# Kernel tuning notes

Hardware: AMD Instinct MI355X
Metric: run time of the kernel (lower is better)

Reference implementation:

```python
import jax, jax.numpy as jnp
import numpy as np

DIM_IN = 768
DIM_OUT = 64
SEQ = 4096
BATCH = 4

def setup_inputs() -> dict:
    key = jax.random.key(0)
    ks = jax.random.split(key, 7)
    s = 1.0 / np.sqrt(DIM_IN)
    return {
        "x": jax.random.normal(ks[0], (BATCH, SEQ, DIM_IN), dtype=jnp.float32),
        "wq": jax.random.uniform(ks[1], (DIM_IN, DIM_OUT), jnp.float32, -s, s),
        "bq": jax.random.uniform(ks[2], (DIM_OUT,), jnp.float32, -s, s),
        "wk": jax.random.uniform(ks[3], (DIM_IN, DIM_OUT), jnp.float32, -s, s),
        "bk": jax.random.uniform(ks[4], (DIM_OUT,), jnp.float32, -s, s),
        "wv": jax.random.uniform(ks[5], (DIM_IN, DIM_OUT), jnp.float32, -s, s),
        "bv": jax.random.uniform(ks[6], (DIM_OUT,), jnp.float32, -s, s),
    }

def reference(x, wq, bq, wk, bk, wv, bv):
    # QKV projections: (B, S, D_in) @ (D_in, D_out) + bias
    q = x @ wq + bq
    k = x @ wk + bk
    v = x @ wv + bv
    # full causal attention, scores scaled by sqrt(d_out) AFTER masking (as in source)
    scores = jnp.einsum('bqd,bkd->bqk', q, k)  # (B, S, S)
    seq = x.shape[1]
    causal = jnp.tril(jnp.ones((seq, seq), dtype=bool))  # True = keep
    scores = jnp.where(causal, scores, -jnp.inf)
    scale = 1.0 / np.sqrt(k.shape[-1]).astype(np.float32)
    weights = jax.nn.softmax(scores * scale, axis=-1)
    # dropout_rate = 0.0 -> identity
    return jnp.einsum('bqk,bkd->bqd', weights, v)
```

## Files before the change

### kernel.cpp

```cpp
#include <hip/hip_runtime.h>
#include <hip/hip_bf16.h>

#define BATCH 4
#define SEQ   4096
#define DIN   768
#define DOUT  64

typedef __attribute__((ext_vector_type(4))) float f32x4;
typedef __attribute__((ext_vector_type(8))) short short8;
typedef __attribute__((ext_vector_type(4))) short short4v;
typedef __attribute__((ext_vector_type(2))) unsigned uint2v;

#define QSCALE 0.18033688011112043f

static __device__ __forceinline__ unsigned short f2bf(float f) {
    union { float f; unsigned u; } un; un.f = f;
    unsigned r = un.u + 0x7FFF + ((un.u >> 16) & 1);
    return (unsigned short)(r >> 16);
}
static __device__ __forceinline__ float bf2f(unsigned short h) {
    union { unsigned u; float f; } un; un.u = ((unsigned)h) << 16;
    return un.f;
}
static __device__ __forceinline__ unsigned packbf(float lo, float hi) {
    return ((unsigned)f2bf(hi) << 16) | (unsigned)f2bf(lo);
}

__global__ void wprep_kernel(const float* __restrict__ wq,
                             const float* __restrict__ wk,
                             const float* __restrict__ wv,
                             unsigned short* __restrict__ wF) {
    __shared__ float lds[64][65];
    int o = blockIdx.x / 12, kt = blockIdx.x % 12;
    const float* w = (o == 0) ? wq : (o == 1) ? wk : wv;
    int tid = threadIdx.x;
    int k0 = kt * 64;
    #pragma unroll
    for (int i = 0; i < 16; ++i) {
        int flat = tid + i * 256;
        int kl = flat >> 6, n = flat & 63;
        lds[kl][n] = w[(k0 + kl) * 64 + n];
    }
    __syncthreads();
    int lane = tid & 63;
    int m = lane & 15, g = lane >> 4;
    #pragma unroll
    for (int i = 0; i < 2; ++i) {
        int f = i * 4 + (tid >> 6);
        int t = f >> 1, kcl = f & 1;
        int kc = kt * 2 + kcl;
        int nc = o * 4 + t;
        short8 v;
        #pragma unroll
        for (int j = 0; j < 8; ++j)
            v[j] = (short)f2bf(lds[kcl * 32 + g * 8 + j][t * 16 + m]);
        *(short8*)&wF[(size_t)(nc * 24 + kc) * 512 + lane * 8] = v;
    }
}

__global__ void __launch_bounds__(256) proj_kernel(
        const float* __restrict__ x,
        const float* __restrict__ bq,
        const float* __restrict__ bk,
        const float* __restrict__ bv,
        const unsigned short* __restrict__ wF,
        unsigned short* __restrict__ Qf,
        unsigned short* __restrict__ Kf,
        unsigned short* __restrict__ Vf) {
    __shared__ __align__(16) unsigned short xs[32][776];
    __shared__ unsigned short tr[4][16][24];

    int tid = threadIdx.x;
    int w = tid >> 6;
    int lane = tid & 63;
    int m = lane & 15, g = lane >> 4;
    int r0 = blockIdx.x * 32;

    {
        const float* xbase = x + (size_t)r0 * DIN;
        #pragma unroll
        for (int i = 0; i < 24; ++i) {
            int flat4 = tid + i * 256;
            int row = flat4 / 192;
            int c4 = flat4 - row * 192;
            float4 v = *(const float4*)(xbase + (size_t)row * DIN + c4 * 4);
            short4v sv;
            sv[0] = (short)f2bf(v.x); sv[1] = (short)f2bf(v.y);
            sv[2] = (short)f2bf(v.z); sv[3] = (short)f2bf(v.w);
            *(short4v*)&xs[row][c4 * 4] = sv;
        }
    }
    __syncthreads();

    f32x4 acc[2][3];
    #pragma unroll
    for (int st = 0; st < 2; ++st)
        #pragma unroll
        for (int t = 0; t < 3; ++t) acc[st][t] = (f32x4){0.f, 0.f, 0.f, 0.f};

    const unsigned short* wb0 = wF + (size_t)((w * 3 + 0) * 24) * 512 + lane * 8;
    const unsigned short* wb1 = wF + (size_t)((w * 3 + 1) * 24) * 512 + lane * 8;
    const unsigned short* wb2 = wF + (size_t)((w * 3 + 2) * 24) * 512 + lane * 8;

    short8 bf0 = *(const short8*)(wb0);
    short8 bf1 = *(const short8*)(wb1);
    short8 bf2 = *(const short8*)(wb2);
    short8 af0 = *(const short8*)&xs[m][g * 8];
    short8 af1 = *(const short8*)&xs[16 + m][g * 8];

    for (int kc = 0; kc < 24; ++kc) {
        short8 nb0, nb1, nb2, na0, na1;
        bool have = (kc + 1) < 24;
        if (have) {
            int off = (kc + 1) * 512;
            nb0 = *(const short8*)(wb0 + off);
            nb1 = *(const short8*)(wb1 + off);
            nb2 = *(const short8*)(wb2 + off);
            na0 = *(const short8*)&xs[m][(kc + 1) * 32 + g * 8];
            na1 = *(const short8*)&xs[16 + m][(kc + 1) * 32 + g * 8];
        }
        acc[0][0] = __builtin_amdgcn_mfma_f32_16x16x32_bf16(af0, bf0, acc[0][0], 0, 0, 0);
        acc[1][0] = __builtin_amdgcn_mfma_f32_16x16x32_bf16(af1, bf0, acc[1][0], 0, 0, 0);
        acc[0][1] = __builtin_amdgcn_mfma_f32_16x16x32_bf16(af0, bf1, acc[0][1], 0, 0, 0);
        acc[1][1] = __builtin_amdgcn_mfma_f32_16x16x32_bf16(af1, bf1, acc[1][1], 0, 0, 0);
        acc[0][2] = __builtin_amdgcn_mfma_f32_16x16x32_bf16(af0, bf2, acc[0][2], 0, 0, 0);
        acc[1][2] = __builtin_amdgcn_mfma_f32_16x16x32_bf16(af1, bf2, acc[1][2], 0, 0, 0);
        if (have) {
            bf0 = nb0; bf1 = nb1; bf2 = nb2;
            af0 = na0; af1 = na1;
        }
    }

    int b2 = r0 >> 12;
    int s = (r0 & 4095) >> 5;
    #pragma unroll
    for (int st = 0; st < 2; ++st) {
        #pragma unroll
        for (int tt = 0; tt < 3; ++tt) {
            int nc = w * 3 + tt;
            int o = nc >> 2;
            int t = nc & 3;
            const float* bias_p = (o == 0) ? bq : (o == 1) ? bk : bv;
            float bias = bias_p[t * 16 + m];
            #pragma unroll
            for (int r = 0; r < 4; ++r) {
                float val = acc[st][tt][r] + bias;
                if (o == 0) val *= QSCALE;
                tr[w][g * 4 + r][m] = f2bf(val);
            }
            if (o < 2) {
                if (g < 2) {
                    short8 v8;
                    #pragma unroll
                    for (int j = 0; j < 8; ++j) v8[j] = (short)tr[w][m][g * 8 + j];
                    unsigned short* dst = (o == 0) ? Qf : Kf;
                    int c = t >> 1;
                    *(short8*)&dst[(size_t)((blockIdx.x * 2 + st) * 2 + c) * 512
                                   + (((t & 1) * 2 + g) * 16 + m) * 8] = v8;
                }
            } else {
                if (g < 2) {
                    short8 v8;
                    #pragma unroll
                    for (int j = 0; j < 8; ++j) v8[j] = (short)tr[w][g * 8 + j][m];
                    *(short8*)&Vf[((size_t)(b2 * 128 + s) * 4 + t) * 512
                                  + ((st * 2 + g) * 16 + m) * 8] = v8;
                }
            }
        }
    }
}

__global__ void __launch_bounds__(512, 1) attn_kernel(
        const unsigned short* __restrict__ Qf,
        const unsigned short* __restrict__ Kf,
        const unsigned short* __restrict__ Vf,
        float* __restrict__ out) {
    __shared__ __align__(16) unsigned short PT[8][16][40];
    __shared__ __align__(16) unsigned short pacc[8][16][68];
    __shared__ float pm[8][16];
    __shared__ float pl[8][16];

    int j = blockIdx.x;
    int b = j & 3;
    int qt = j >> 2;
    int T[4];
    T[0] = qt; T[1] = 127 - qt; T[2] = 128 + qt; T[3] = 255 - qt;
    int ns[4], base[4];
    #pragma unroll
    for (int i = 0; i < 4; ++i) { base[i] = T[i] * 16; ns[i] = (T[i] + 2) >> 1; }
    int tid = threadIdx.x;
    int w = tid >> 6;
    int lane = tid & 63;
    int m = lane & 15, g = lane >> 4;

    short8 qfr[4][2];
    #pragma unroll
    for (int i = 0; i < 4; ++i) {
        const unsigned short* Qp = Qf + (size_t)(b * 256 + T[i]) * 1024 + lane * 8;
        qfr[i][0] = *(const short8*)(Qp);
        qfr[i][1] = *(const short8*)(Qp + 512);
    }

    short8 onesA;
    #pragma unroll
    for (int jj = 0; jj < 8; ++jj) onesA[jj] = (short)0x3F80;

    f32x4 acc[4][5];
    #pragma unroll
    for (int rt = 0; rt < 4; ++rt)
        #pragma unroll
        for (int t = 0; t < 5; ++t) acc[rt][t] = (f32x4){0.f, 0.f, 0.f, 0.f};
    float mrun[4];
    #pragma unroll
    for (int rt = 0; rt < 4; ++rt) mrun[rt] = -INFINITY;

    const unsigned short* Kbase = Kf + (size_t)(b * 256) * 1024 + lane * 8;
    const unsigned short* Vbase = Vf + (size_t)(b * 128) * 2048 + lane * 8;

    short8 kf[4], vf[4];
    if (w < ns[3]) {
        #pragma unroll
        for (int t = 0; t < 4; ++t) {
            kf[t] = *(const short8*)(Kbase + (size_t)w * 2048 + t * 512);
            vf[t] = *(const short8*)(Vbase + (size_t)w * 2048 + t * 512);
        }
    }

    for (int s = w; s < ns[3]; s += 8) {
        int kv0 = s * 32;
        int sn = s + 8;
        bool have = (sn < ns[3]);

        #pragma unroll
        for (int rt = 0; rt < 4; ++rt) {
            if (rt < 3 && s >= ns[rt]) continue;

            f32x4 st0 = (f32x4){0.f, 0.f, 0.f, 0.f};
            f32x4 st1 = (f32x4){0.f, 0.f, 0.f, 0.f};
            st0 = __builtin_amdgcn_mfma_f32_16x16x32_bf16(kf[0], qfr[rt][0], st0, 0, 0, 0);
            st0 = __builtin_amdgcn_mfma_f32_16x16x32_bf16(kf[1], qfr[rt][1], st0, 0, 0, 0);
            st1 = __builtin_amdgcn_mfma_f32_16x16x32_bf16(kf[2], qfr[rt][0], st1, 0, 0, 0);
            st1 = __builtin_amdgcn_mfma_f32_16x16x32_bf16(kf[3], qfr[rt][1], st1, 0, 0, 0);

            if (rt == 3 && have) {
                #pragma unroll
                for (int t = 0; t < 4; ++t)
                    kf[t] = *(const short8*)(Kbase + (size_t)sn * 2048 + t * 512);
            }

            if (s == ns[rt] - 1) {
                int q = base[rt] + m;
                #pragma unroll
                for (int r = 0; r < 4; ++r) {
                    if (kv0 + g * 4 + r > q)      st0[r] = -INFINITY;
                    if (kv0 + 16 + g * 4 + r > q) st1[r] = -INFINITY;
                }
            }

            float th = mrun[rt] + 8.0f;
            bool need = (st0[0] > th) | (st0[1] > th) | (st0[2] > th) | (st0[3] > th)
                      | (st1[0] > th) | (st1[1] > th) | (st1[2] > th) | (st1[3] > th);
            if (__any(need)) {
                float rmax = fmaxf(fmaxf(fmaxf(st0[0], st0[1]), fmaxf(st0[2], st0[3])),
                                   fmaxf(fmaxf(st1[0], st1[1]), fmaxf(st1[2], st1[3])));
                rmax = fmaxf(rmax, __shfl_xor(rmax, 16));
                rmax = fmaxf(rmax, __shfl_xor(rmax, 32));
                float mnew = fmaxf(mrun[rt], rmax);
                float alpha = __builtin_amdgcn_exp2f(mrun[rt] - mnew);
                mrun[rt] = mnew;
                #pragma unroll
                for (int t = 0; t < 5; ++t)
                    #pragma unroll
                    for (int r = 0; r < 4; ++r) acc[rt][t][r] *= alpha;
            }
            float p00 = __builtin_amdgcn_exp2f(st0[0] - mrun[rt]);
            float p01 = __builtin_amdgcn_exp2f(st0[1] - mrun[rt]);
            float p02 = __builtin_amdgcn_exp2f(st0[2] - mrun[rt]);
            float p03 = __builtin_amdgcn_exp2f(st0[3] - mrun[rt]);
            float p10 = __builtin_amdgcn_exp2f(st1[0] - mrun[rt]);
            float p11 = __builtin_amdgcn_exp2f(st1[1] - mrun[rt]);
            float p12 = __builtin_amdgcn_exp2f(st1[2] - mrun[rt]);
            float p13 = __builtin_amdgcn_exp2f(st1[3] - mrun[rt]);
            *(uint2v*)&PT[w][m][g * 4]      = (uint2v){packbf(p00, p01), packbf(p02, p03)};
            *(uint2v*)&PT[w][m][16 + g * 4] = (uint2v){packbf(p10, p11), packbf(p12, p13)};
            short8 pb = *(const short8*)&PT[w][m][g * 8];
            #pragma unroll
            for (int t = 0; t < 4; ++t)
                acc[rt][t] = __builtin_amdgcn_mfma_f32_16x16x32_bf16(vf[t], pb, acc[rt][t], 0, 0, 0);
            acc[rt][4] = __builtin_amdgcn_mfma_f32_16x16x32_bf16(onesA, pb, acc[rt][4], 0, 0, 0);
        }

        if (have) {
            #pragma unroll
            for (int t = 0; t < 4; ++t)
                vf[t] = *(const short8*)(Vbase + (size_t)sn * 2048 + t * 512);
        }
    }

    #pragma unroll
    for (int rt = 0; rt < 4; ++rt) {
        if (lane < 16) {
            pm[w][m] = mrun[rt];
            pl[w][m] = acc[rt][4][0];
        }
        #pragma unroll
        for (int t = 0; t < 4; ++t)
            #pragma unroll
            for (int r = 0; r < 4; ++r)
                pacc[w][m][t * 16 + g * 4 + r] = f2bf(acc[rt][t][r]);
        __syncthreads();

        if (tid < 256) {
            int row = tid >> 4;
            int c4 = (tid & 15) * 4;
            float mmax = pm[0][row];
            #pragma unroll
            for (int w2 = 1; w2 < 8; ++w2) mmax = fmaxf(mmax, pm[w2][row]);
            float lt = 0.f;
            float o0 = 0.f, o1 = 0.f, o2 = 0.f, o3 = 0.f;
            #pragma unroll
            for (int w2 = 0; w2 < 8; ++w2) {
                float sc2 = __builtin_amdgcn_exp2f(pm[w2][row] - mmax);
                lt += pl[w2][row] * sc2;
                short4v pa4 = *(const short4v*)&pacc[w2][row][c4];
                o0 += bf2f((unsigned short)pa4[0]) * sc2;
                o1 += bf2f((unsigned short)pa4[1]) * sc2;
                o2 += bf2f((unsigned short)pa4[2]) * sc2;
                o3 += bf2f((unsigned short)pa4[3]) * sc2;
            }
            float invl = 1.0f / lt;
            float4 res = make_float4(o0 * invl, o1 * invl, o2 * invl, o3 * invl);
            *(float4*)&out[(size_t)(b * SEQ + base[rt] + row) * DOUT + c4] = res;
        }
        __syncthreads();
    }
}

extern "C" void kernel_launch(void* const* d_in, const int* in_sizes, int n_in,
                              void* d_out, int out_size, void* d_ws, size_t ws_size,
                              hipStream_t stream) {
    const float* x  = (const float*)d_in[0];
    const float* wq = (const float*)d_in[1];
    const float* bq = (const float*)d_in[2];
    const float* wk = (const float*)d_in[3];
    const float* bk = (const float*)d_in[4];
    const float* wv = (const float*)d_in[5];
    const float* bv = (const float*)d_in[6];
    float* out = (float*)d_out;

    char* ws = (char*)d_ws;
    unsigned short* wF = (unsigned short*)ws;
    unsigned short* Qf = (unsigned short*)(ws + 294912);
    unsigned short* Kf = (unsigned short*)(ws + 294912 + 2097152);
    unsigned short* Vf = (unsigned short*)(ws + 294912 + 4194304);

    wprep_kernel<<<36, 256, 0, stream>>>(wq, wk, wv, wF);
    proj_kernel<<<512, 256, 0, stream>>>(x, bq, bk, bv, wF, Qf, Kf, Vf);
    attn_kernel<<<256, 512, 0, stream>>>(Qf, Kf, Vf, out);
}
```

Before: 49.19 us.

## Split attention into one query tile per block with 64-wide KV steps

```diff
diff --git a/kernel.cpp b/kernel.cpp
--- a/kernel.cpp
+++ b/kernel.cpp
@@ -67,19 +67,19 @@
         unsigned short* __restrict__ Qf,
         unsigned short* __restrict__ Kf,
         unsigned short* __restrict__ Vf) {
-    __shared__ __align__(16) unsigned short xs[32][776];
+    __shared__ __align__(16) unsigned short xs[16][776];
     __shared__ unsigned short tr[4][16][24];
 
     int tid = threadIdx.x;
     int w = tid >> 6;
     int lane = tid & 63;
     int m = lane & 15, g = lane >> 4;
-    int r0 = blockIdx.x * 32;
+    int r0 = blockIdx.x * 16;
 
     {
         const float* xbase = x + (size_t)r0 * DIN;
         #pragma unroll
-        for (int i = 0; i < 24; ++i) {
+        for (int i = 0; i < 12; ++i) {
             int flat4 = tid + i * 256;
             int row = flat4 / 192;
             int c4 = flat4 - row * 192;
@@ -92,11 +92,9 @@
     }
     __syncthreads();
 
-    f32x4 acc[2][3];
-    #pragma unroll
-    for (int st = 0; st < 2; ++st)
-        #pragma unroll
-        for (int t = 0; t < 3; ++t) acc[st][t] = (f32x4){0.f, 0.f, 0.f, 0.f};
+    f32x4 acc[3];
+    #pragma unroll
+    for (int t = 0; t < 3; ++t) acc[t] = (f32x4){0.f, 0.f, 0.f, 0.f};
 
     const unsigned short* wb0 = wF + (size_t)((w * 3 + 0) * 24) * 512 + lane * 8;
     const unsigned short* wb1 = wF + (size_t)((w * 3 + 1) * 24) * 512 + lane * 8;
@@ -106,10 +104,9 @@
     short8 bf1 = *(const short8*)(wb1);
     short8 bf2 = *(const short8*)(wb2);
     short8 af0 = *(const short8*)&xs[m][g * 8];
-    short8 af1 = *(const short8*)&xs[16 + m][g * 8];
 
     for (int kc = 0; kc < 24; ++kc) {
-        short8 nb0, nb1, nb2, na0, na1;
+        short8 nb0, nb1, nb2, na0;
         bool have = (kc + 1) < 24;
         if (have) {
             int off = (kc + 1) * 512;
@@ -117,223 +114,215 @@
             nb1 = *(const short8*)(wb1 + off);
             nb2 = *(const short8*)(wb2 + off);
             na0 = *(const short8*)&xs[m][(kc + 1) * 32 + g * 8];
-            na1 = *(const short8*)&xs[16 + m][(kc + 1) * 32 + g * 8];
-        }
-        acc[0][0] = __builtin_amdgcn_mfma_f32_16x16x32_bf16(af0, bf0, acc[0][0], 0, 0, 0);
-        acc[1][0] = __builtin_amdgcn_mfma_f32_16x16x32_bf16(af1, bf0, acc[1][0], 0, 0, 0);
-        acc[0][1] = __builtin_amdgcn_mfma_f32_16x16x32_bf16(af0, bf1, acc[0][1], 0, 0, 0);
-        acc[1][1] = __builtin_amdgcn_mfma_f32_16x16x32_bf16(af1, bf1, acc[1][1], 0, 0, 0);
-        acc[0][2] = __builtin_amdgcn_mfma_f32_16x16x32_bf16(af0, bf2, acc[0][2], 0, 0, 0);
-        acc[1][2] = __builtin_amdgcn_mfma_f32_16x16x32_bf16(af1, bf2, acc[1][2], 0, 0, 0);
+        }
+        acc[0] = __builtin_amdgcn_mfma_f32_16x16x32_bf16(af0, bf0, acc[0], 0, 0, 0);
+        acc[1] = __builtin_amdgcn_mfma_f32_16x16x32_bf16(af0, bf1, acc[1], 0, 0, 0);
+        acc[2] = __builtin_amdgcn_mfma_f32_16x16x32_bf16(af0, bf2, acc[2], 0, 0, 0);
         if (have) {
-            bf0 = nb0; bf1 = nb1; bf2 = nb2;
-            af0 = na0; af1 = na1;
+            bf0 = nb0; bf1 = nb1; bf2 = nb2; af0 = na0;
         }
     }
 
     int b2 = r0 >> 12;
-    int s = (r0 & 4095) >> 5;
-    #pragma unroll
-    for (int st = 0; st < 2; ++st) {
-        #pragma unroll
-        for (int tt = 0; tt < 3; ++tt) {
-            int nc = w * 3 + tt;
-            int o = nc >> 2;
-            int t = nc & 3;
-            const float* bias_p = (o == 0) ? bq : (o == 1) ? bk : bv;
-            float bias = bias_p[t * 16 + m];
-            #pragma unroll
-            for (int r = 0; r < 4; ++r) {
-                float val = acc[st][tt][r] + bias;
-                if (o == 0) val *= QSCALE;
-                tr[w][g * 4 + r][m] = f2bf(val);
+    int ss = r0 & 4095;
+    int s = ss >> 5, half = (ss >> 4) & 1;
+    #pragma unroll
+    for (int tt = 0; tt < 3; ++tt) {
+        int nc = w * 3 + tt;
+        int o = nc >> 2;
+        int t = nc & 3;
+        const float* bias_p = (o == 0) ? bq : (o == 1) ? bk : bv;
+        float bias = bias_p[t * 16 + m];
+        #pragma unroll
+        for (int r = 0; r < 4; ++r) {
+            float val = acc[tt][r] + bias;
+            if (o == 0) val *= QSCALE;
+            tr[w][g * 4 + r][m] = f2bf(val);
+        }
+        if (o < 2) {
+            if (g < 2) {
+                short8 v8;
+                #pragma unroll
+                for (int j = 0; j < 8; ++j) v8[j] = (short)tr[w][m][g * 8 + j];
+                unsigned short* dst = (o == 0) ? Qf : Kf;
+                int c = t >> 1;
+                *(short8*)&dst[(size_t)(blockIdx.x * 2 + c) * 512
+                               + (((t & 1) * 2 + g) * 16 + m) * 8] = v8;
             }
-            if (o < 2) {
-                if (g < 2) {
-                    short8 v8;
-                    #pragma unroll
-                    for (int j = 0; j < 8; ++j) v8[j] = (short)tr[w][m][g * 8 + j];
-                    unsigned short* dst = (o == 0) ? Qf : Kf;
-                    int c = t >> 1;
-                    *(short8*)&dst[(size_t)((blockIdx.x * 2 + st) * 2 + c) * 512
-                                   + (((t & 1) * 2 + g) * 16 + m) * 8] = v8;
-                }
-            } else {
-                if (g < 2) {
-                    short8 v8;
-                    #pragma unroll
-                    for (int j = 0; j < 8; ++j) v8[j] = (short)tr[w][g * 8 + j][m];
-                    *(short8*)&Vf[((size_t)(b2 * 128 + s) * 4 + t) * 512
-                                  + ((st * 2 + g) * 16 + m) * 8] = v8;
-                }
+        } else {
+            if (g < 2) {
+                short8 v8;
+                #pragma unroll
+                for (int j = 0; j < 8; ++j) v8[j] = (short)tr[w][g * 8 + j][m];
+                *(short8*)&Vf[((size_t)(b2 * 128 + s) * 4 + t) * 512
+                              + ((half * 2 + g) * 16 + m) * 8] = v8;
             }
         }
     }
 }
 
-__global__ void __launch_bounds__(512, 1) attn_kernel(
+__global__ void __launch_bounds__(512, 2) attn_kernel(
         const unsigned short* __restrict__ Qf,
         const unsigned short* __restrict__ Kf,
         const unsigned short* __restrict__ Vf,
         float* __restrict__ out) {
-    __shared__ __align__(16) unsigned short PT[8][16][40];
+    __shared__ __align__(16) unsigned short PT[8][16][72];
     __shared__ __align__(16) unsigned short pacc[8][16][68];
     __shared__ float pm[8][16];
     __shared__ float pl[8][16];
 
     int j = blockIdx.x;
     int b = j & 3;
-    int qt = j >> 2;
-    int T[4];
-    T[0] = qt; T[1] = 127 - qt; T[2] = 128 + qt; T[3] = 255 - qt;
-    int ns[4], base[4];
-    #pragma unroll
-    for (int i = 0; i < 4; ++i) { base[i] = T[i] * 16; ns[i] = (T[i] + 2) >> 1; }
+    int qt = 255 - (j >> 2);
+    int q0 = qt * 16;
+    int ns = (q0 + 79) >> 6;
     int tid = threadIdx.x;
     int w = tid >> 6;
     int lane = tid & 63;
     int m = lane & 15, g = lane >> 4;
 
-    short8 qfr[4][2];
-    #pragma unroll
-    for (int i = 0; i < 4; ++i) {
-        const unsigned short* Qp = Qf + (size_t)(b * 256 + T[i]) * 1024 + lane * 8;
-        qfr[i][0] = *(const short8*)(Qp);
-        qfr[i][1] = *(const short8*)(Qp + 512);
-    }
+    const unsigned short* Qp = Qf + (size_t)(b * 256 + qt) * 1024 + lane * 8;
+    short8 qf0 = *(const short8*)(Qp);
+    short8 qf1 = *(const short8*)(Qp + 512);
 
     short8 onesA;
     #pragma unroll
     for (int jj = 0; jj < 8; ++jj) onesA[jj] = (short)0x3F80;
 
-    f32x4 acc[4][5];
-    #pragma unroll
-    for (int rt = 0; rt < 4; ++rt)
-        #pragma unroll
-        for (int t = 0; t < 5; ++t) acc[rt][t] = (f32x4){0.f, 0.f, 0.f, 0.f};
-    float mrun[4];
-    #pragma unroll
-    for (int rt = 0; rt < 4; ++rt) mrun[rt] = -INFINITY;
+    f32x4 acc[5];
+    #pragma unroll
+    for (int t = 0; t < 5; ++t) acc[t] = (f32x4){0.f, 0.f, 0.f, 0.f};
+    float mrun = -INFINITY;
 
     const unsigned short* Kbase = Kf + (size_t)(b * 256) * 1024 + lane * 8;
     const unsigned short* Vbase = Vf + (size_t)(b * 128) * 2048 + lane * 8;
 
-    short8 kf[4], vf[4];
-    if (w < ns[3]) {
+    short8 kf[8], vf[8];
+    if (w < ns) {
+        #pragma unroll
+        for (int u = 0; u < 4; ++u) {
+            kf[2 * u]     = *(const short8*)(Kbase + (size_t)w * 4096 + u * 1024);
+            kf[2 * u + 1] = *(const short8*)(Kbase + (size_t)w * 4096 + u * 1024 + 512);
+        }
+        #pragma unroll
+        for (int c = 0; c < 2; ++c)
+            #pragma unroll
+            for (int t = 0; t < 4; ++t)
+                vf[c * 4 + t] = *(const short8*)(Vbase + (size_t)(2 * w + c) * 2048 + t * 512);
+    }
+
+    for (int s = w; s < ns; s += 8) {
+        int kv0 = s * 64;
+        int sn = s + 8;
+        bool have = (sn < ns);
+
+        f32x4 st[4];
+        #pragma unroll
+        for (int u = 0; u < 4; ++u) {
+            st[u] = (f32x4){0.f, 0.f, 0.f, 0.f};
+            st[u] = __builtin_amdgcn_mfma_f32_16x16x32_bf16(kf[2 * u],     qf0, st[u], 0, 0, 0);
+            st[u] = __builtin_amdgcn_mfma_f32_16x16x32_bf16(kf[2 * u + 1], qf1, st[u], 0, 0, 0);
+        }
+
+        if (have) {
+            #pragma unroll
+            for (int u = 0; u < 4; ++u) {
+                kf[2 * u]     = *(const short8*)(Kbase + (size_t)sn * 4096 + u * 1024);
+                kf[2 * u + 1] = *(const short8*)(Kbase + (size_t)sn * 4096 + u * 1024 + 512);
+            }
+        }
+
+        if (s == ns - 1) {
+            int q = q0 + m;
+            #pragma unroll
+            for (int u = 0; u < 4; ++u)
+                #pragma unroll
+                for (int r = 0; r < 4; ++r)
+                    if (kv0 + u * 16 + g * 4 + r > q) st[u][r] = -INFINITY;
+        }
+
+        float th = mrun + 8.0f;
+        bool need = false;
+        #pragma unroll
+        for (int u = 0; u < 4; ++u)
+            need = need | (st[u][0] > th) | (st[u][1] > th)
+                        | (st[u][2] > th) | (st[u][3] > th);
+        if (__any(need)) {
+            float rmax = -INFINITY;
+            #pragma unroll
+            for (int u = 0; u < 4; ++u)
+                rmax = fmaxf(rmax, fmaxf(fmaxf(st[u][0], st[u][1]), fmaxf(st[u][2], st[u][3])));
+            rmax = fmaxf(rmax, __shfl_xor(rmax, 16));
+            rmax = fmaxf(rmax, __shfl_xor(rmax, 32));
+            float mnew = fmaxf(mrun, rmax);
+            float alpha = __builtin_amdgcn_exp2f(mrun - mnew);
+            mrun = mnew;
+            #pragma unroll
+            for (int t = 0; t < 5; ++t)
+                #pragma unroll
+                for (int r = 0; r < 4; ++r) acc[t][r] *= alpha;
+        }
+
+        #pragma unroll
+        for (int u = 0; u < 4; ++u) {
+            float e0 = __builtin_amdgcn_exp2f(st[u][0] - mrun);
+            float e1 = __builtin_amdgcn_exp2f(st[u][1] - mrun);
+            float e2 = __builtin_amdgcn_exp2f(st[u][2] - mrun);
+            float e3 = __builtin_amdgcn_exp2f(st[u][3] - mrun);
+            *(uint2v*)&PT[w][m][u * 16 + g * 4] = (uint2v){packbf(e0, e1), packbf(e2, e3)};
+        }
+        short8 pb0 = *(const short8*)&PT[w][m][g * 8];
+        short8 pb1 = *(const short8*)&PT[w][m][32 + g * 8];
+
         #pragma unroll
         for (int t = 0; t < 4; ++t) {
-            kf[t] = *(const short8*)(Kbase + (size_t)w * 2048 + t * 512);
-            vf[t] = *(const short8*)(Vbase + (size_t)w * 2048 + t * 512);
-        }
-    }
-
-    for (int s = w; s < ns[3]; s += 8) {
-        int kv0 = s * 32;
-        int sn = s + 8;
-        bool have = (sn < ns[3]);
-
-        #pragma unroll
-        for (int rt = 0; rt < 4; ++rt) {
-            if (rt < 3 && s >= ns[rt]) continue;
-
-            f32x4 st0 = (f32x4){0.f, 0.f, 0.f, 0.f};
-            f32x4 st1 = (f32x4){0.f, 0.f, 0.f, 0.f};
-            st0 = __builtin_amdgcn_mfma_f32_16x16x32_bf16(kf[0], qfr[rt][0], st0, 0, 0, 0);
-            st0 = __builtin_amdgcn_mfma_f32_16x16x32_bf16(kf[1], qfr[rt][1], st0, 0, 0, 0);
-            st1 = __builtin_amdgcn_mfma_f32_16x16x32_bf16(kf[2], qfr[rt][0], st1, 0, 0, 0);
-            st1 = __builtin_amdgcn_mfma_f32_16x16x32_bf16(kf[3], qfr[rt][1], st1, 0, 0, 0);
-
-            if (rt == 3 && have) {
+            acc[t] = __builtin_amdgcn_mfma_f32_16x16x32_bf16(vf[t],     pb0, acc[t], 0, 0, 0);
+            acc[t] = __builtin_amdgcn_mfma_f32_16x16x32_bf16(vf[4 + t], pb1, acc[t], 0, 0, 0);
+        }
+        acc[4] = __builtin_amdgcn_mfma_f32_16x16x32_bf16(onesA, pb0, acc[4], 0, 0, 0);
+        acc[4] = __builtin_amdgcn_mfma_f32_16x16x32_bf16(onesA, pb1, acc[4], 0, 0, 0);
+
+        if (have) {
+            #pragma unroll
+            for (int c = 0; c < 2; ++c)
                 #pragma unroll
                 for (int t = 0; t < 4; ++t)
-                    kf[t] = *(const short8*)(Kbase + (size_t)sn * 2048 + t * 512);
-            }
-
-            if (s == ns[rt] - 1) {
-                int q = base[rt] + m;
-                #pragma unroll
-                for (int r = 0; r < 4; ++r) {
-                    if (kv0 + g * 4 + r > q)      st0[r] = -INFINITY;
-                    if (kv0 + 16 + g * 4 + r > q) st1[r] = -INFINITY;
-                }
-            }
-
-            float th = mrun[rt] + 8.0f;
-            bool need = (st0[0] > th) | (st0[1] > th) | (st0[2] > th) | (st0[3] > th)
-                      | (st1[0] > th) | (st1[1] > th) | (st1[2] > th) | (st1[3] > th);
-            if (__any(need)) {
-                float rmax = fmaxf(fmaxf(fmaxf(st0[0], st0[1]), fmaxf(st0[2], st0[3])),
-                                   fmaxf(fmaxf(st1[0], st1[1]), fmaxf(st1[2], st1[3])));
-                rmax = fmaxf(rmax, __shfl_xor(rmax, 16));
-                rmax = fmaxf(rmax, __shfl_xor(rmax, 32));
-                float mnew = fmaxf(mrun[rt], rmax);
-                float alpha = __builtin_amdgcn_exp2f(mrun[rt] - mnew);
-                mrun[rt] = mnew;
-                #pragma unroll
-                for (int t = 0; t < 5; ++t)
-                    #pragma unroll
-                    for (int r = 0; r < 4; ++r) acc[rt][t][r] *= alpha;
-            }
-            float p00 = __builtin_amdgcn_exp2f(st0[0] - mrun[rt]);
-            float p01 = __builtin_amdgcn_exp2f(st0[1] - mrun[rt]);
-            float p02 = __builtin_amdgcn_exp2f(st0[2] - mrun[rt]);
-            float p03 = __builtin_amdgcn_exp2f(st0[3] - mrun[rt]);
-            float p10 = __builtin_amdgcn_exp2f(st1[0] - mrun[rt]);
-            float p11 = __builtin_amdgcn_exp2f(st1[1] - mrun[rt]);
-            float p12 = __builtin_amdgcn_exp2f(st1[2] - mrun[rt]);
-            float p13 = __builtin_amdgcn_exp2f(st1[3] - mrun[rt]);
-            *(uint2v*)&PT[w][m][g * 4]      = (uint2v){packbf(p00, p01), packbf(p02, p03)};
-            *(uint2v*)&PT[w][m][16 + g * 4] = (uint2v){packbf(p10, p11), packbf(p12, p13)};
-            short8 pb = *(const short8*)&PT[w][m][g * 8];
-            #pragma unroll
-            for (int t = 0; t < 4; ++t)
-                acc[rt][t] = __builtin_amdgcn_mfma_f32_16x16x32_bf16(vf[t], pb, acc[rt][t], 0, 0, 0);
-            acc[rt][4] = __builtin_amdgcn_mfma_f32_16x16x32_bf16(onesA, pb, acc[rt][4], 0, 0, 0);
-        }
-
-        if (have) {
-            #pragma unroll
-            for (int t = 0; t < 4; ++t)
-                vf[t] = *(const short8*)(Vbase + (size_t)sn * 2048 + t * 512);
-        }
-    }
-
-    #pragma unroll
-    for (int rt = 0; rt < 4; ++rt) {
-        if (lane < 16) {
-            pm[w][m] = mrun[rt];
-            pl[w][m] = acc[rt][4][0];
-        }
-        #pragma unroll
-        for (int t = 0; t < 4; ++t)
-            #pragma unroll
-            for (int r = 0; r < 4; ++r)
-                pacc[w][m][t * 16 + g * 4 + r] = f2bf(acc[rt][t][r]);
-        __syncthreads();
-
-        if (tid < 256) {
-            int row = tid >> 4;
-            int c4 = (tid & 15) * 4;
-            float mmax = pm[0][row];
-            #pragma unroll
-            for (int w2 = 1; w2 < 8; ++w2) mmax = fmaxf(mmax, pm[w2][row]);
-            float lt = 0.f;
-            float o0 = 0.f, o1 = 0.f, o2 = 0.f, o3 = 0.f;
-            #pragma unroll
-            for (int w2 = 0; w2 < 8; ++w2) {
-                float sc2 = __builtin_amdgcn_exp2f(pm[w2][row] - mmax);
-                lt += pl[w2][row] * sc2;
-                short4v pa4 = *(const short4v*)&pacc[w2][row][c4];
-                o0 += bf2f((unsigned short)pa4[0]) * sc2;
-                o1 += bf2f((unsigned short)pa4[1]) * sc2;
-                o2 += bf2f((unsigned short)pa4[2]) * sc2;
-                o3 += bf2f((unsigned short)pa4[3]) * sc2;
-            }
-            float invl = 1.0f / lt;
-            float4 res = make_float4(o0 * invl, o1 * invl, o2 * invl, o3 * invl);
-            *(float4*)&out[(size_t)(b * SEQ + base[rt] + row) * DOUT + c4] = res;
-        }
-        __syncthreads();
+                    vf[c * 4 + t] = *(const short8*)(Vbase + (size_t)(2 * sn + c) * 2048 + t * 512);
+        }
+    }
+
+    if (lane < 16) {
+        pm[w][m] = mrun;
+        pl[w][m] = acc[4][0];
+    }
+    #pragma unroll
+    for (int t = 0; t < 4; ++t)
+        #pragma unroll
+        for (int r = 0; r < 4; ++r)
+            pacc[w][m][t * 16 + g * 4 + r] = f2bf(acc[t][r]);
+    __syncthreads();
+
+    if (tid < 256) {
+        int row = tid >> 4;
+        int c4 = (tid & 15) * 4;
+        float mmax = pm[0][row];
+        #pragma unroll
+        for (int w2 = 1; w2 < 8; ++w2) mmax = fmaxf(mmax, pm[w2][row]);
+        float lt = 0.f;
+        float o0 = 0.f, o1 = 0.f, o2 = 0.f, o3 = 0.f;
+        #pragma unroll
+        for (int w2 = 0; w2 < 8; ++w2) {
+            float sc2 = __builtin_amdgcn_exp2f(pm[w2][row] - mmax);
+            lt += pl[w2][row] * sc2;
+            short4v pa4 = *(const short4v*)&pacc[w2][row][c4];
+            o0 += bf2f((unsigned short)pa4[0]) * sc2;
+            o1 += bf2f((unsigned short)pa4[1]) * sc2;
+            o2 += bf2f((unsigned short)pa4[2]) * sc2;
+            o3 += bf2f((unsigned short)pa4[3]) * sc2;
+        }
+        float invl = 1.0f / lt;
+        float4 res = make_float4(o0 * invl, o1 * invl, o2 * invl, o3 * invl);
+        *(float4*)&out[(size_t)(b * SEQ + q0 + row) * DOUT + c4] = res;
     }
 }
 
@@ -356,6 +345,6 @@
     unsigned short* Vf = (unsigned short*)(ws + 294912 + 4194304);
 
     wprep_kernel<<<36, 256, 0, stream>>>(wq, wk, wv, wF);
-    proj_kernel<<<512, 256, 0, stream>>>(x, bq, bk, bv, wF, Qf, Kf, Vf);
-    attn_kernel<<<256, 512, 0, stream>>>(Qf, Kf, Vf, out);
-}
+    proj_kernel<<<1024, 256, 0, stream>>>(x, bq, bk, bv, wF, Qf, Kf, Vf);
+    attn_kernel<<<1024, 512, 0, stream>>>(Qf, Kf, Vf, out);
+}
```

Result: slower. 52.80 us (+7.3%).
